# Performance work log

Hardware: AMD Instinct MI355X
Metric: run time of the kernel (lower is better)

The kernel has to match this reference:

```python
import jax, jax.numpy as jnp
import numpy as np

D_MODEL = 1024
N_HEAD = 16
D_HEAD = D_MODEL // N_HEAD
FFN_HIDDEN = 4096
NEG_INF = -1e30


def sinusoid_pos_emb(pos_seq, d_model):
    # pos_seq: [K] descending relative positions; returns [K, d_model]
    inv_freq = 1.0 / (10000.0 ** (jnp.arange(0, d_model, 2, dtype=jnp.float32) / d_model))
    ang = pos_seq[:, None] * inv_freq[None, :]
    return jnp.concatenate([jnp.sin(ang), jnp.cos(ang)], axis=-1)


def rel_shift(x):
    # x: [B, H, Q, K] -> Transformer-XL relative shift
    b, h, q, k = x.shape
    x = jnp.pad(x, ((0, 0), (0, 0), (0, 0), (1, 0)))
    x = x.reshape(b, h, k + 1, q)[:, :, 1:, :].reshape(b, h, q, k)
    return x


def layer_norm(x, g, b, eps=1e-5):
    mu = jnp.mean(x, axis=-1, keepdims=True)
    var = jnp.var(x, axis=-1, keepdims=True)
    return (x - mu) * jax.lax.rsqrt(var + eps) * g + b


def setup_inputs() -> dict:
    key = jax.random.key(0)
    ks = jax.random.split(key, 20)
    B, T, M = 4, 2048, 2048
    s = 0.02
    inp = {
        "x": jax.random.normal(ks[0], (B, T, D_MODEL), jnp.float32),
        "mem": jax.random.normal(ks[1], (B, M, D_MODEL), jnp.float32),
        "Wq": jax.random.normal(ks[2], (D_MODEL, D_MODEL), jnp.float32) * s,
        "bq": jnp.zeros((D_MODEL,), jnp.float32),
        "Wk": jax.random.normal(ks[3], (D_MODEL, D_MODEL), jnp.float32) * s,
        "bk": jnp.zeros((D_MODEL,), jnp.float32),
        "Wv": jax.random.normal(ks[4], (D_MODEL, D_MODEL), jnp.float32) * s,
        "bv": jnp.zeros((D_MODEL,), jnp.float32),
        "Wo": jax.random.normal(ks[5], (D_MODEL, D_MODEL), jnp.float32) * s,
        "bo": jnp.zeros((D_MODEL,), jnp.float32),
        "Wr": jax.random.normal(ks[6], (D_MODEL, D_MODEL), jnp.float32) * s,
        "u": jax.random.normal(ks[7], (N_HEAD, D_HEAD), jnp.float32) * s,
        "v": jax.random.normal(ks[8], (N_HEAD, D_HEAD), jnp.float32) * s,
        "g1": jnp.ones((D_MODEL,), jnp.float32),
        "be1": jnp.zeros((D_MODEL,), jnp.float32),
        "g2": jnp.ones((D_MODEL,), jnp.float32),
        "be2": jnp.zeros((D_MODEL,), jnp.float32),
        "W1": jax.random.normal(ks[9], (D_MODEL, FFN_HIDDEN), jnp.float32) * s,
        "b1": jnp.zeros((FFN_HIDDEN,), jnp.float32),
        "W2": jax.random.normal(ks[10], (FFN_HIDDEN, D_MODEL), jnp.float32) * s,
        "b2": jnp.zeros((D_MODEL,), jnp.float32),
        "is_causal": 1,
    }
    return inp


def xl_attention(x, mem, Wq, bq, Wk, bk, Wv, bv, Wo, bo, Wr, u, v, is_causal):
    B, T, D = x.shape
    M = mem.shape[1]
    K = M + T
    c = jnp.concatenate([mem, x], axis=1)  # [B, K, D]
    q = (x @ Wq + bq).reshape(B, T, N_HEAD, D_HEAD)
    k = (c @ Wk + bk).reshape(B, K, N_HEAD, D_HEAD)
    vv = (c @ Wv + bv).reshape(B, K, N_HEAD, D_HEAD)
    pos_seq = jnp.arange(K - 1, -1, -1, dtype=jnp.float32)
    r = (sinusoid_pos_emb(pos_seq, D) @ Wr).reshape(K, N_HEAD, D_HEAD)
    # content term + relative-position term (Transformer-XL eq. A+C and B+D)
    AC = jnp.einsum('bihd,bjhd->bhij', q + u, k)
    BD = rel_shift(jnp.einsum('bihd,jhd->bhij', q + v, r))
    score = (AC + BD) * (1.0 / np.sqrt(D_HEAD))
    if is_causal:
        i = jnp.arange(T)[:, None]
        j = jnp.arange(K)[None, :]
        causal = (j <= i + M)  # query i may attend keys up to its own position
        score = jnp.where(causal[None, None], score, NEG_INF)
    attn = jax.nn.softmax(score, axis=-1)
    out = jnp.einsum('bhij,bjhd->bihd', attn, vv).reshape(B, T, D)
    return out @ Wo + bo


def reference(x, mem, Wq, bq, Wk, bk, Wv, bv, Wo, bo, Wr, u, v,
              g1, be1, g2, be2, W1, b1, W2, b2, is_causal):
    # dropout is identity at inference
    a = xl_attention(x, mem, Wq, bq, Wk, bk, Wv, bv, Wo, bo, Wr, u, v, is_causal)
    h = layer_norm(a + x, g1, be1)
    f = jax.nn.gelu(h @ W1 + b1) @ W2 + b2
    return layer_norm(f + h, g2, be2)
```

## Files before the change

kernel.cpp:

```cpp
#include <hip/hip_runtime.h>
#include <stdint.h>

typedef unsigned short u16;
typedef short s16x8 __attribute__((ext_vector_type(8)));
typedef unsigned short u16x4 __attribute__((ext_vector_type(4)));
typedef float f32x4 __attribute__((ext_vector_type(4)));

#define DEV static __device__ __forceinline__

DEV u16 f2b(float f) {
  union { float f; unsigned u; } v; v.f = f;
  unsigned r = v.u + 0x7fffu + ((v.u >> 16) & 1u);
  return (u16)(r >> 16);
}
DEV float b2f(u16 b) {
  union { unsigned u; float f; } v; v.u = ((unsigned)b) << 16; return v.f;
}
DEV unsigned pk_trunc(float a, float b) {
  return __builtin_amdgcn_perm(__float_as_uint(b), __float_as_uint(a), 0x07060302u);
}
DEV f32x4 MFMA16(s16x8 a, s16x8 b, f32x4 c) {
  return __builtin_amdgcn_mfma_f32_16x16x32_bf16(a, b, c, 0, 0, 0);
}
#define GLD_LDS16(gp, lp)                                                            \
  __builtin_amdgcn_global_load_lds((const __attribute__((address_space(1))) void*)(gp), \
                                   (__attribute__((address_space(3))) void*)(lp), 16, 0, 0)


__global__ __launch_bounds__(256) void wt_cast_t(const float* __restrict__ W,
                                                 u16* __restrict__ Wt, int Kd, int Nd) {
  __shared__ float tile[32][33];
  const int n0 = blockIdx.x * 32, k0 = blockIdx.y * 32;
  const int t = threadIdx.x;
#pragma unroll
  for (int p = 0; p < 4; ++p) {
    int idx = p * 256 + t; int r = idx >> 5, c = idx & 31;
    tile[r][c] = W[(long)(k0 + r) * Nd + n0 + c];
  }
  __syncthreads();
#pragma unroll
  for (int p = 0; p < 4; ++p) {
    int idx = p * 256 + t; int r = idx >> 5, c = idx & 31;
    Wt[(long)(n0 + r) * Kd + k0 + c] = f2b(tile[c][r]);
  }
}

__global__ __launch_bounds__(256) void build_cb(const float* __restrict__ x,
                                                const float* __restrict__ mem,
                                                u16* __restrict__ cb) {
  long idx = (long)blockIdx.x * 256 + threadIdx.x;
  long e4 = idx * 4;
  int b = (int)(e4 >> 22);
  long rem = e4 & ((1L << 22) - 1);
  int tok = (int)(rem >> 10);
  int d = (int)(rem & 1023);
  const float* src = (tok < 2048) ? &mem[((long)b * 2048 + tok) * 1024 + d]
                                  : &x[((long)b * 2048 + (tok - 2048)) * 1024 + d];
  float4 vv = *(const float4*)src;
  uint2 o;
  o.x = (unsigned)f2b(vv.x) | ((unsigned)f2b(vv.y) << 16);
  o.y = (unsigned)f2b(vv.z) | ((unsigned)f2b(vv.w) << 16);
  *(uint2*)&cb[e4] = o;
}

__global__ __launch_bounds__(256) void pos_emb(u16* __restrict__ pe) {
  const int d = blockIdx.x;
  const int e0 = threadIdx.x * 4;
  u16 o[4];
#pragma unroll
  for (int i = 0; i < 4; ++i) {
    int e = e0 + i;
    int f = (e < 512) ? e : (e - 512);
    float invf = expf(-(float)f * (9.210340371976184f / 512.f));
    float ang = (float)d * invf;
    o[i] = f2b((e < 512) ? sinf(ang) : cosf(ang));
  }
  uint2 pk; pk.x = (unsigned)o[0] | ((unsigned)o[1] << 16);
  pk.y = (unsigned)o[2] | ((unsigned)o[3] << 16);
  *(uint2*)&pe[(long)d * 1024 + e0] = pk;
}

#define EPI_BF16 0
#define EPI_F32 1
#define EPI_GELU 2
#define EPI_VT 3

template <int EPI, int QMAP>
__global__ __launch_bounds__(256) void gemm_bt(const u16* __restrict__ A,
                                               const u16* __restrict__ Bt,
                                               const float* __restrict__ bias,
                                               void* __restrict__ outp, int Ndim, int Kdim) {
  __shared__ __align__(16) u16 As[128 * 64];
  __shared__ __align__(16) u16 Bs[128 * 64];
  const int col0 = blockIdx.x * 128;
  const int row0 = blockIdx.y * 128;
  const int t = threadIdx.x;
  const int w = t >> 6, l = t & 63;
  const int wr = (w >> 1) * 64, wc = (w & 1) * 64;
  const int lr = l & 15, g = l >> 4;
  f32x4 acc[4][4];
#pragma unroll
  for (int m = 0; m < 4; ++m)
#pragma unroll
    for (int n = 0; n < 4; ++n) acc[m][n] = f32x4{0.f, 0.f, 0.f, 0.f};

  for (int k0 = 0; k0 < Kdim; k0 += 64) {
#pragma unroll
    for (int it = 0; it < 4; ++it) {
      int c = it * 256 + t;
      int r = c >> 3, ch = (c & 7) ^ (r & 7);
      long ga = row0 + r;
      if (QMAP) ga = ((ga >> 11) << 12) + 2048 + (ga & 2047);
      GLD_LDS16(A + ga * Kdim + k0 + ch * 8, &As[c * 8]);
      GLD_LDS16(Bt + (long)(col0 + r) * Kdim + k0 + ch * 8, &Bs[c * 8]);
    }
    __syncthreads();
#pragma unroll
    for (int kk = 0; kk < 2; ++kk) {
      s16x8 af[4], bfv[4];
#pragma unroll
      for (int m = 0; m < 4; ++m) {
        int rm = wr + m * 16 + lr;
        af[m] = *(const s16x8*)&As[rm * 64 + (((g + 4 * kk) ^ (rm & 7)) << 3)];
      }
#pragma unroll
      for (int n = 0; n < 4; ++n) {
        int rn = wc + n * 16 + lr;
        bfv[n] = *(const s16x8*)&Bs[rn * 64 + (((g + 4 * kk) ^ (rn & 7)) << 3)];
      }
#pragma unroll
      for (int m = 0; m < 4; ++m)
#pragma unroll
        for (int n = 0; n < 4; ++n) acc[m][n] = MFMA16(af[m], bfv[n], acc[m][n]);
    }
    __syncthreads();
  }

  const int lg = g * 4;
#pragma unroll
  for (int m = 0; m < 4; ++m) {
    int rbase = row0 + wr + m * 16 + lg;
#pragma unroll
    for (int n = 0; n < 4; ++n) {
      int gc = col0 + wc + n * 16 + lr;
      float bv = bias ? bias[gc] : 0.f;
#pragma unroll
      for (int rg = 0; rg < 4; ++rg) {
        int grow = rbase + rg;
        float vv = acc[m][n][rg] + bv;
        if (EPI == EPI_GELU) {
          float x3 = vv * vv * vv;
          vv = 0.5f * vv * (1.f + tanhf(0.7978845608028654f * (vv + 0.044715f * x3)));
        }
        if (EPI == EPI_F32) {
          ((float*)outp)[(long)grow * Ndim + gc] = vv;
        } else if (EPI == EPI_VT) {
          int bb = grow >> 12, tok = grow & 4095;
          int hh = gc >> 6, dd = gc & 63;
          ((u16*)outp)[((long)((bb * 16 + hh) * 64 + dd) << 12) + tok] = f2b(vv);
        } else {
          ((u16*)outp)[(long)grow * Ndim + gc] = f2b(vv);
        }
      }
    }
  }
}

#define SCALE_LOG2 0.18033688011111793f

__global__ __launch_bounds__(1024, 4) void attn_fused(
    const u16* __restrict__ qg, const u16* __restrict__ kg, const u16* __restrict__ vTg,
    const u16* __restrict__ rg, const float* __restrict__ u, const float* __restrict__ vparam,
    const int* __restrict__ causal_p, u16* __restrict__ Og) {
  __shared__ __align__(16) u16 Ks[2][64 * 64];
  __shared__ __align__(16) u16 Vs[2][64 * 64];
  __shared__ __align__(16) u16 GPs[16][16 * 84];

  const int bh = blockIdx.x, b = bh >> 4, h = bh & 15;
  const int i0 = (int)(gridDim.y - 1 - blockIdx.y) * 256;
  const int t = threadIdx.x, w = t >> 6, l = t & 63;
  const int q = l & 15, g = l >> 4, lk = g * 8;
  const int causal = causal_p[0];

  const long kbase = ((long)b * 4096) * 1024 + h * 64;
  const long vbase = ((long)((b * 16 + h) * 64)) * 4096;

  const int irow = i0 + 16 * w + q;
  const u16* qp = qg + ((long)(b * 2048 + irow)) * 1024 + h * 64;
  s16x8 qlo = *(const s16x8*)(qp + lk);
  s16x8 qhi = *(const s16x8*)(qp + 32 + lk);
  s16x8 qu0, qu1, qv0, qv1;
#pragma unroll
  for (int j = 0; j < 8; ++j) {
    float a0 = b2f((u16)qlo[j]), a1 = b2f((u16)qhi[j]);
    float uu0 = u[h * 64 + lk + j], vv0 = vparam[h * 64 + lk + j];
    float uu1 = u[h * 64 + 32 + lk + j], vv1 = vparam[h * 64 + 32 + lk + j];
    qu0[j] = (short)f2b((a0 + uu0) * SCALE_LOG2); qv0[j] = (short)f2b((a0 + vv0) * SCALE_LOG2);
    qu1[j] = (short)f2b((a1 + uu1) * SCALE_LOG2); qv1[j] = (short)f2b((a1 + vv1) * SCALE_LOG2);
  }

  float lsum = 0.f;
  f32x4 oacc[4];
#pragma unroll
  for (int n = 0; n < 4; ++n) oacc[n] = f32x4{0.f, 0.f, 0.f, 0.f};

  u16* gpw = &GPs[w][0];
  const int kc0 = q * 64 + ((g ^ (q & 7)) << 3);
  const int kc1 = kc0 ^ 32;
  const int gq = q * 85 + 63;
  const int gst = q * 84 + 4 * g;
  const int pst = q * 72 + 4 * g;
  const int prd = q * 72 + lk;

  auto STAGE = [&](int j0s, int bufi) {
    int t9 = t & 511;
    int rrow = t9 >> 3, gch = (t9 & 7) ^ (rrow & 7);
    if (t < 512) GLD_LDS16(kg + kbase + (long)(j0s + rrow) * 1024 + gch * 8, &Ks[bufi][t9 * 8]);
    else         GLD_LDS16(vTg + vbase + (long)rrow * 4096 + j0s + gch * 8, &Vs[bufi][t9 * 8]);
  };

  s16x8 rf0[5], rf1[5];
  auto LOADR = [&](int j0r) {
    const int dlo = 2048 + i0 + 16 * w - j0r - 63;
#pragma unroll
    for (int tt = 0; tt < 5; ++tt) {
      int d = dlo + tt * 16 + q; d = min(max(d, 0), 4095);
      const u16* rp = rg + ((long)d << 10) + h * 64;
      rf0[tt] = *(const s16x8*)(rp + lk);
      rf1[tt] = *(const s16x8*)(rp + 32 + lk);
    }
  };

  const int jmax = causal ? (2048 + i0 + 256) : 4096;
  const int nt = jmax >> 6;
  const int jlimit = 2048 + i0 + 16 * w + 15;

  STAGE(0, 0);
  LOADR(0);
  int cur = 0;

  for (int ti = 0; ti < nt; ++ti) {
    const int j0 = ti << 6;
    __syncthreads();
    if (ti + 1 < nt) STAGE((ti + 1) << 6, cur ^ 1);

    if (!causal || j0 <= jlimit) {
      const u16* ksp = &Ks[cur][0];
      const u16* vsp = &Vs[cur][0];

      f32x4 sv[4];
      __builtin_amdgcn_s_setprio(1);
#pragma unroll
      for (int n = 0; n < 4; ++n) {
        s16x8 af0 = *(const s16x8*)&ksp[kc0 + n * 1024];
        s16x8 af1 = *(const s16x8*)&ksp[kc1 + n * 1024];
        f32x4 z = f32x4{0.f, 0.f, 0.f, 0.f};
        z = MFMA16(af0, qu0, z);
        z = MFMA16(af1, qu1, z);
        sv[n] = z;
      }
#pragma unroll
      for (int tt = 0; tt < 5; ++tt) {
        f32x4 z = f32x4{0.f, 0.f, 0.f, 0.f};
        z = MFMA16(rf0[tt], qv0, z);
        z = MFMA16(rf1[tt], qv1, z);
        uint2 gp2 = {pk_trunc(z[0], z[1]), pk_trunc(z[2], z[3])};
        *(u16x4*)&gpw[gst + tt * 16] = __builtin_bit_cast(u16x4, gp2);
      }
      __builtin_amdgcn_s_setprio(0);

      if (ti + 1 < nt && (!causal || j0 + 64 <= jlimit)) LOADR(j0 + 64);

      const bool need_mask = (causal != 0) && (j0 + 63 > 2048 + i0 + 16 * w);
#pragma unroll
      for (int n = 0; n < 4; ++n) {
#pragma unroll
        for (int r = 0; r < 4; ++r) {
          int j = 16 * n + 4 * g + r;
          float bd = b2f(gpw[gq - j]);
          float scv = sv[n][r] + bd;
          if (need_mask && (j0 + j > 2048 + irow)) scv = -3.0e38f;
          sv[n][r] = scv;
        }
      }
      float ls = 0.f;
#pragma unroll
      for (int n = 0; n < 4; ++n) {
        float p0 = __builtin_amdgcn_exp2f(sv[n][0]);
        float p1 = __builtin_amdgcn_exp2f(sv[n][1]);
        float p2 = __builtin_amdgcn_exp2f(sv[n][2]);
        float p3 = __builtin_amdgcn_exp2f(sv[n][3]);
        ls += (p0 + p1) + (p2 + p3);
        uint2 pp = {pk_trunc(p0, p1), pk_trunc(p2, p3)};
        *(u16x4*)&gpw[pst + n * 16] = __builtin_bit_cast(u16x4, pp);
      }
      lsum += ls;

      s16x8 pb0 = *(const s16x8*)&gpw[prd];
      s16x8 pb1 = *(const s16x8*)&gpw[prd + 32];
      __builtin_amdgcn_s_setprio(1);
#pragma unroll
      for (int n = 0; n < 4; ++n) {
        s16x8 va0 = *(const s16x8*)&vsp[kc0 + n * 1024];
        s16x8 va1 = *(const s16x8*)&vsp[kc1 + n * 1024];
        oacc[n] = MFMA16(va0, pb0, oacc[n]);
        oacc[n] = MFMA16(va1, pb1, oacc[n]);
      }
      __builtin_amdgcn_s_setprio(0);
    }
    cur ^= 1;
  }

  lsum += __shfl_xor(lsum, 16);
  lsum += __shfl_xor(lsum, 32);
  const float linv = 1.f / lsum;
  const long obase = (long)(b * 2048 + irow) * 1024 + h * 64;
#pragma unroll
  for (int n = 0; n < 4; ++n) {
    u16x4 ov = {f2b(oacc[n][0] * linv), f2b(oacc[n][1] * linv),
                f2b(oacc[n][2] * linv), f2b(oacc[n][3] * linv)};
    *(u16x4*)&Og[obase + n * 16 + 4 * g] = ov;
  }
}

template <int WRITE_BF16>
__global__ __launch_bounds__(256) void ln_res(const float* __restrict__ a,
                                              const float* __restrict__ resid,
                                              const float* __restrict__ g,
                                              const float* __restrict__ be,
                                              float* __restrict__ outf, u16* __restrict__ outb) {
  const int row = blockIdx.x;
  const int t = threadIdx.x;
  const long base = (long)row * 1024;
  float4 av = *(const float4*)&a[base + t * 4];
  float4 rv = *(const float4*)&resid[base + t * 4];
  float x0 = av.x + rv.x, x1 = av.y + rv.y, x2 = av.z + rv.z, x3 = av.w + rv.w;
  float s = x0 + x1 + x2 + x3;
  float q = x0 * x0 + x1 * x1 + x2 * x2 + x3 * x3;
#pragma unroll
  for (int d = 1; d < 64; d <<= 1) {
    s += __shfl_xor(s, d);
    q += __shfl_xor(q, d);
  }
  __shared__ float ss[4], sq[4];
  if ((t & 63) == 0) { ss[t >> 6] = s; sq[t >> 6] = q; }
  __syncthreads();
  s = ss[0] + ss[1] + ss[2] + ss[3];
  q = sq[0] + sq[1] + sq[2] + sq[3];
  float mu = s * (1.f / 1024.f);
  float var = q * (1.f / 1024.f) - mu * mu;
  float rstd = rsqrtf(var + 1e-5f);
  float4 gv = *(const float4*)&g[t * 4];
  float4 bv = *(const float4*)&be[t * 4];
  float y0 = (x0 - mu) * rstd * gv.x + bv.x;
  float y1 = (x1 - mu) * rstd * gv.y + bv.y;
  float y2 = (x2 - mu) * rstd * gv.z + bv.z;
  float y3 = (x3 - mu) * rstd * gv.w + bv.w;
  float4 ov = {y0, y1, y2, y3};
  *(float4*)&outf[base + t * 4] = ov;
  if (WRITE_BF16) {
    uint2 o;
    o.x = (unsigned)f2b(y0) | ((unsigned)f2b(y1) << 16);
    o.y = (unsigned)f2b(y2) | ((unsigned)f2b(y3) << 16);
    *(uint2*)&outb[base + t * 4] = o;
  }
}

extern "C" void kernel_launch(void* const* d_in, const int* in_sizes, int n_in, void* d_out,
                              int out_size, void* d_ws, size_t ws_size, hipStream_t stream) {
  const float* x = (const float*)d_in[0];
  const float* mem = (const float*)d_in[1];
  const float* Wq = (const float*)d_in[2];
  const float* bq = (const float*)d_in[3];
  const float* Wk = (const float*)d_in[4];
  const float* bk = (const float*)d_in[5];
  const float* Wv = (const float*)d_in[6];
  const float* bv = (const float*)d_in[7];
  const float* Wo = (const float*)d_in[8];
  const float* bo = (const float*)d_in[9];
  const float* Wr = (const float*)d_in[10];
  const float* u = (const float*)d_in[11];
  const float* vp = (const float*)d_in[12];
  const float* g1 = (const float*)d_in[13];
  const float* be1 = (const float*)d_in[14];
  const float* g2 = (const float*)d_in[15];
  const float* be2 = (const float*)d_in[16];
  const float* W1 = (const float*)d_in[17];
  const float* b1 = (const float*)d_in[18];
  const float* W2 = (const float*)d_in[19];
  const float* b2 = (const float*)d_in[20];
  const int* iscaus = (const int*)d_in[21];

  char* ws = (char*)d_ws;
  const size_t MB = 1024 * 1024;
  u16* WqT = (u16*)(ws + 0 * MB);
  u16* WkT = (u16*)(ws + 2 * MB);
  u16* WvT = (u16*)(ws + 4 * MB);
  u16* WoT = (u16*)(ws + 6 * MB);
  u16* WrT = (u16*)(ws + 8 * MB);
  u16* W1T = (u16*)(ws + 10 * MB);
  u16* W2T = (u16*)(ws + 18 * MB);
  u16* cb = (u16*)(ws + 26 * MB);
  float* proj = (float*)(ws + 26 * MB);
  u16* pe = (u16*)(ws + 58 * MB);
  u16* qb = (u16*)(ws + 66 * MB);
  u16* kb = (u16*)(ws + 82 * MB);
  u16* vT = (u16*)(ws + 114 * MB);
  u16* rb = (u16*)(ws + 146 * MB);
  u16* aO = (u16*)(ws + 154 * MB);
  u16* hb = (u16*)(ws + 154 * MB);
  u16* f1 = (u16*)(ws + 58 * MB);
  float* f2 = (float*)(ws + 122 * MB);
  (void)ws_size; (void)in_sizes; (void)n_in; (void)out_size;

  wt_cast_t<<<dim3(32, 32), 256, 0, stream>>>(Wq, WqT, 1024, 1024);
  wt_cast_t<<<dim3(32, 32), 256, 0, stream>>>(Wk, WkT, 1024, 1024);
  wt_cast_t<<<dim3(32, 32), 256, 0, stream>>>(Wv, WvT, 1024, 1024);
  wt_cast_t<<<dim3(32, 32), 256, 0, stream>>>(Wo, WoT, 1024, 1024);
  wt_cast_t<<<dim3(32, 32), 256, 0, stream>>>(Wr, WrT, 1024, 1024);
  wt_cast_t<<<dim3(128, 32), 256, 0, stream>>>(W1, W1T, 1024, 4096);
  wt_cast_t<<<dim3(32, 128), 256, 0, stream>>>(W2, W2T, 4096, 1024);

  build_cb<<<16384, 256, 0, stream>>>(x, mem, cb);
  pos_emb<<<4096, 256, 0, stream>>>(pe);

  gemm_bt<EPI_BF16, 1><<<dim3(8, 64), 256, 0, stream>>>(cb, WqT, bq, qb, 1024, 1024);
  gemm_bt<EPI_BF16, 0><<<dim3(8, 128), 256, 0, stream>>>(cb, WkT, bk, kb, 1024, 1024);
  gemm_bt<EPI_VT, 0><<<dim3(8, 128), 256, 0, stream>>>(cb, WvT, bv, vT, 1024, 1024);
  gemm_bt<EPI_BF16, 0><<<dim3(8, 32), 256, 0, stream>>>(pe, WrT, nullptr, rb, 1024, 1024);

  attn_fused<<<dim3(64, 8), 1024, 0, stream>>>(qb, kb, vT, rb, u, vp, iscaus, aO);

  gemm_bt<EPI_F32, 0><<<dim3(8, 64), 256, 0, stream>>>(aO, WoT, bo, proj, 1024, 1024);
  ln_res<1><<<8192, 256, 0, stream>>>(proj, x, g1, be1, proj, hb);

  gemm_bt<EPI_GELU, 0><<<dim3(32, 64), 256, 0, stream>>>(hb, W1T, b1, f1, 4096, 1024);
  gemm_bt<EPI_F32, 0><<<dim3(8, 64), 256, 0, stream>>>(f1, W2T, b2, f2, 1024, 4096);
  ln_res<0><<<8192, 256, 0, stream>>>(f2, proj, g2, be2, (float*)d_out, nullptr);
}
```

Measured before the change: 954.1 us.

## Add 256-row double-buffered GEMM kernel with interleaved prefetch for projections and FFN

Adds a new gemm_big kernel that uses 512-thread blocks and 256xBN tiles (BN of 128 or 256) with double-buffered LDS. It interleaves global-to-LDS prefetch of the next K tile with the MFMA phases and raises wave priority around the MFMA bursts. The Q/K/V, output projection and both FFN GEMMs now use it, aiming for more data reuse per block and better overlap of loads with compute. The larger tiles need more LDS and registers, which can lower occupancy, and the bigger blocks leave fewer of them to fill the CUs.

```diff
diff --git a/kernel.cpp b/kernel.cpp
--- a/kernel.cpp
+++ b/kernel.cpp
@@ -142,6 +142,112 @@
     int rbase = row0 + wr + m * 16 + lg;
 #pragma unroll
     for (int n = 0; n < 4; ++n) {
+      int gc = col0 + wc + n * 16 + lr;
+      float bv = bias ? bias[gc] : 0.f;
+#pragma unroll
+      for (int rg = 0; rg < 4; ++rg) {
+        float vv = acc[m][n][rg] + bv;
+        ((u16*)outp)[(long)(rbase + rg) * Ndim + gc] = f2b(vv);
+      }
+    }
+  }
+}
+
+template <int EPI, int QMAP, int BN>
+__global__ __launch_bounds__(512) void gemm_big(const u16* __restrict__ A,
+                                                const u16* __restrict__ Bt,
+                                                const float* __restrict__ bias,
+                                                void* __restrict__ outp, int Ndim, int Kdim) {
+  constexpr int NF = BN / 64;
+  __shared__ __align__(16) u16 As[2][256 * 64];
+  __shared__ __align__(16) u16 Bs[2][BN * 64];
+  const int col0 = blockIdx.x * BN;
+  const int row0 = blockIdx.y * 256;
+  const int t = threadIdx.x;
+  const int w = t >> 6, l = t & 63;
+  const int wr = (w >> 2) * 128, wc = (w & 3) * (BN / 4);
+  const int lr = l & 15, g = l >> 4;
+
+  f32x4 acc[8][NF];
+#pragma unroll
+  for (int m = 0; m < 8; ++m)
+#pragma unroll
+    for (int n = 0; n < NF; ++n) acc[m][n] = f32x4{0.f, 0.f, 0.f, 0.f};
+
+  auto stageA = [&](int k0, int p, int nb) {
+    int c = p * 512 + t;
+    int r = c >> 3, ch = (c & 7) ^ (r & 7);
+    long ga = row0 + r;
+    if (QMAP) ga = ((ga >> 11) << 12) + 2048 + (ga & 2047);
+    GLD_LDS16(A + ga * Kdim + k0 + ch * 8, &As[nb][c * 8]);
+  };
+  auto stageB = [&](int k0, int p, int nb) {
+    int c = p * 512 + t;
+    int r = c >> 3, ch = (c & 7) ^ (r & 7);
+    GLD_LDS16(Bt + (long)(col0 + r) * Kdim + k0 + ch * 8, &Bs[nb][c * 8]);
+  };
+
+  const int nt = Kdim >> 6;
+#pragma unroll
+  for (int p = 0; p < 4; ++p) stageA(0, p, 0);
+#pragma unroll
+  for (int p = 0; p < NF; ++p) stageB(0, p, 0);
+  __syncthreads();
+  int cur = 0;
+
+  for (int ti = 0; ti < nt; ++ti) {
+    const int k1 = (ti + 1) << 6;
+    const int nb = cur ^ 1;
+    s16x8 bf[NF][2];
+#pragma unroll
+    for (int p = 0; p < 4; ++p) {
+      s16x8 af[2][2];
+#pragma unroll
+      for (int i = 0; i < 2; ++i) {
+        int rm = wr + (2 * p + i) * 16 + lr;
+#pragma unroll
+        for (int kk = 0; kk < 2; ++kk)
+          af[i][kk] = *(const s16x8*)&As[cur][rm * 64 + (((g + 4 * kk) ^ (rm & 7)) << 3)];
+      }
+      if (p == 0) {
+#pragma unroll
+        for (int n = 0; n < NF; ++n) {
+          int rn = wc + n * 16 + lr;
+#pragma unroll
+          for (int kk = 0; kk < 2; ++kk)
+            bf[n][kk] = *(const s16x8*)&Bs[cur][rn * 64 + (((g + 4 * kk) ^ (rn & 7)) << 3)];
+        }
+      }
+      if (ti + 1 < nt) {
+        if (p == 0) { stageA(k1, 0, nb); stageB(k1, 0, nb); }
+        else if (p == 1) { stageA(k1, 1, nb); if (NF > 1) stageB(k1, 1, nb); }
+        else if (p == 2) {
+          stageA(k1, 2, nb); stageA(k1, 3, nb);
+          if (NF == 4) { stageB(k1, 2, nb); stageB(k1, 3, nb); }
+        }
+      }
+      __builtin_amdgcn_s_barrier();
+      __builtin_amdgcn_s_setprio(1);
+#pragma unroll
+      for (int i = 0; i < 2; ++i)
+#pragma unroll
+        for (int n = 0; n < NF; ++n) {
+          acc[2 * p + i][n] = MFMA16(af[i][0], bf[n][0], acc[2 * p + i][n]);
+          acc[2 * p + i][n] = MFMA16(af[i][1], bf[n][1], acc[2 * p + i][n]);
+        }
+      __builtin_amdgcn_s_setprio(0);
+      if (p < 3) __builtin_amdgcn_s_barrier();
+    }
+    __syncthreads();
+    cur ^= 1;
+  }
+
+  const int lg = g * 4;
+#pragma unroll
+  for (int m = 0; m < 8; ++m) {
+    int rbase = row0 + wr + m * 16 + lg;
+#pragma unroll
+    for (int n = 0; n < NF; ++n) {
       int gc = col0 + wc + n * 16 + lr;
       float bv = bias ? bias[gc] : 0.f;
 #pragma unroll
@@ -424,17 +530,17 @@
   build_cb<<<16384, 256, 0, stream>>>(x, mem, cb);
   pos_emb<<<4096, 256, 0, stream>>>(pe);
 
-  gemm_bt<EPI_BF16, 1><<<dim3(8, 64), 256, 0, stream>>>(cb, WqT, bq, qb, 1024, 1024);
-  gemm_bt<EPI_BF16, 0><<<dim3(8, 128), 256, 0, stream>>>(cb, WkT, bk, kb, 1024, 1024);
-  gemm_bt<EPI_VT, 0><<<dim3(8, 128), 256, 0, stream>>>(cb, WvT, bv, vT, 1024, 1024);
+  gemm_big<EPI_BF16, 1, 128><<<dim3(8, 32), 512, 0, stream>>>(cb, WqT, bq, qb, 1024, 1024);
+  gemm_big<EPI_BF16, 0, 256><<<dim3(4, 64), 512, 0, stream>>>(cb, WkT, bk, kb, 1024, 1024);
+  gemm_big<EPI_VT, 0, 256><<<dim3(4, 64), 512, 0, stream>>>(cb, WvT, bv, vT, 1024, 1024);
   gemm_bt<EPI_BF16, 0><<<dim3(8, 32), 256, 0, stream>>>(pe, WrT, nullptr, rb, 1024, 1024);
 
   attn_fused<<<dim3(64, 8), 1024, 0, stream>>>(qb, kb, vT, rb, u, vp, iscaus, aO);
 
-  gemm_bt<EPI_F32, 0><<<dim3(8, 64), 256, 0, stream>>>(aO, WoT, bo, proj, 1024, 1024);
+  gemm_big<EPI_F32, 0, 128><<<dim3(8, 32), 512, 0, stream>>>(aO, WoT, bo, proj, 1024, 1024);
   ln_res<1><<<8192, 256, 0, stream>>>(proj, x, g1, be1, proj, hb);
 
-  gemm_bt<EPI_GELU, 0><<<dim3(32, 64), 256, 0, stream>>>(hb, W1T, b1, f1, 4096, 1024);
-  gemm_bt<EPI_F32, 0><<<dim3(8, 64), 256, 0, stream>>>(f1, W2T, b2, f2, 1024, 4096);
+  gemm_big<EPI_GELU, 0, 256><<<dim3(16, 32), 512, 0, stream>>>(hb, W1T, b1, f1, 4096, 1024);
+  gemm_big<EPI_F32, 0, 128><<<dim3(8, 32), 512, 0, stream>>>(f1, W2T, b2, f2, 1024, 4096);
   ln_res<0><<<8192, 256, 0, stream>>>(f2, proj, g2, be2, (float*)d_out, nullptr);
 }
```

New measurement: 911.7 us. -4.4%, faster.
